# Optimization experiments

Measured on AMD Instinct MI355X. Metric: run time of the kernel, lower is better.

## Reference

```python
import jax, jax.numpy as jnp
import numpy as np

B, T, D, H, W = 128, 1024, 32, 64, 128
C = D + 1            # control_size = data_size + 1
O = H * C            # cvf MLP output size


def _linear_params(k, out_f, in_f):
    lim = 1.0 / np.sqrt(in_f)
    kw, kb = jax.random.split(k)
    Wm = jax.random.uniform(kw, (out_f, in_f), minval=-lim, maxval=lim, dtype=jnp.float32)
    b = jax.random.uniform(kb, (out_f,), minval=-lim, maxval=lim, dtype=jnp.float32)
    return Wm, b


def setup_inputs() -> dict:
    key = jax.random.key(0)
    ks = jax.random.split(key, 8)
    # initial MLP: (D+1) -> W -> W -> H, relu hidden
    iW0, ib0 = _linear_params(ks[0], W, D + 1)
    iW1, ib1 = _linear_params(ks[1], W, W)
    iW2, ib2 = _linear_params(ks[2], H, W)
    # cvf MLP: (H+1) -> W -> W -> H*C, lipswish hidden, tanh final
    vW0, vb0 = _linear_params(ks[3], W, H + 1)
    vW1, vb1 = _linear_params(ks[4], W, W)
    vW2, vb2 = _linear_params(ks[5], O, W)
    # readout: H -> 1
    rW, rb = _linear_params(ks[6], 1, H)
    ts = jnp.arange(T, dtype=jnp.float32)
    ys = jax.random.normal(ks[7], (B, T, D), dtype=jnp.float32)
    return dict(ts=ts, ys=ys,
                iW0=iW0, ib0=ib0, iW1=iW1, ib1=ib1, iW2=iW2, ib2=ib2,
                vW0=vW0, vb0=vb0, vW1=vb1 * 0 + vW1, vb1=vb1, vW2=vW2, vb2=vb2,
                rW=rW, rb=rb)


def _lipswish(x):
    return 0.909 * jax.nn.silu(x)


def reference(ts, ys, iW0, ib0, iW1, ib1, iW2, ib2,
              vW0, vb0, vW1, vb1, vW2, vb2, rW, rb):
    b, t_len, d = ys.shape
    h = iW2.shape[0]
    c = d + 1

    def initial_mlp(x):  # [B, D+1] -> [B, H]
        z = jax.nn.relu(x @ iW0.T + ib0)
        z = jax.nn.relu(z @ iW1.T + ib1)
        return z @ iW2.T + ib2

    def vf(t, y):  # scalar t, y [B,H] -> [B,H,C]
        inp = jnp.concatenate([jnp.full((y.shape[0], 1), t, y.dtype), y], axis=1)
        z = _lipswish(inp @ vW0.T + vb0)
        z = _lipswish(z @ vW1.T + vb1)
        out = jnp.tanh(z @ vW2.T + vb2)
        return out.reshape(y.shape[0], h, c)

    # control path values x(t_i) = [t_i, y_i]; no NaNs so interpolation fixups are no-ops
    xs = jnp.concatenate([jnp.broadcast_to(ts[None, :, None], (b, t_len, 1)), ys], axis=2)  # [B,T,C]
    y0 = initial_mlp(xs[:, 0])
    vf0 = vf(ts[0], y0)

    # constant step dt=1 aligned with grid -> control increments are consecutive diffs
    dxs = jnp.swapaxes(xs[:, 1:] - xs[:, :-1], 0, 1)  # [T-1,B,C]
    t1s = ts[1:]

    def step(carry, inp):
        y, yhat, v = carry
        t1, dx = inp
        # ReversibleHeun: yhat1 = 2*y - yhat + f(t0,yhat0)·dx ; y1 = y + 0.5*(f0+f1)·dx
        yhat1 = 2.0 * y - yhat + jnp.einsum('bhc,bc->bh', v, dx)
        v1 = vf(t1, yhat1)
        y1 = y + 0.5 * jnp.einsum('bhc,bc->bh', v + v1, dx)
        return (y1, yhat1, v1), None

    (yT, _, _), _ = jax.lax.scan(step, (y0, y0, vf0), (t1s, dxs))
    return yT @ rW.T + rb  # [B,1]
```

## Files before the change

### kernel.cpp

```cpp
#include <hip/hip_runtime.h>
#include <math.h>

constexpr int kB  = 128;
constexpr int kT  = 1024;
constexpr int kD  = 32;
constexpr int kH  = 64;
constexpr int kW  = 128;
constexpr int kC  = kD + 1;
constexpr int kO  = kH * kC;
constexpr int kIN = kH + 1;
constexpr int BLOCK = 1024;

constexpr int WS_W2  = 0;
constexpr int WS_W1  = 135168;
constexpr int WS_W0  = 143360;
constexpr int WS_SC2 = 147584;
constexpr int WS_SC1 = 149696;
constexpr int WS_SC0 = 149824;
constexpr int WS_TOT = 149952;

__device__ __forceinline__ float fast_sigmoid(float x) { return 1.0f / (1.0f + __expf(-x)); }
__device__ __forceinline__ float lipswish_f(float x)   { return 0.909f * x * fast_sigmoid(x); }
__device__ __forceinline__ float fast_tanh(float x) {
    float ax = fabsf(x);
    float e  = __expf(2.0f * ax);
    float r  = 1.0f - 2.0f / (e + 1.0f);
    return copysignf(r, x);
}
__device__ __forceinline__ float dot4(float4 a, float4 b) {
    return a.x * b.x + a.y * b.y + a.z * b.z + a.w * b.w;
}
__device__ __forceinline__ float fma2i(unsigned u, float z0, float z1, float acc) {
    int lo = (int)(short)(u & 0xffffu);
    int hi = ((int)u) >> 16;
    acc += (float)lo * z0 + (float)hi * z1;
    return acc;
}
__device__ __forceinline__ float fma8i(uint4 u, float4 zl, float4 zh, float acc) {
    acc = fma2i(u.x, zl.x, zl.y, acc);
    acc = fma2i(u.y, zl.z, zl.w, acc);
    acc = fma2i(u.z, zh.x, zh.y, acc);
    acc = fma2i(u.w, zh.z, zh.w, acc);
    return acc;
}
__device__ __forceinline__ int q15(float w, float inv) {
    float q = rintf(w * inv);
    q = fmaxf(-32767.0f, fminf(32767.0f, q));
    return (int)q;
}
__device__ __forceinline__ unsigned pack16(int a, int b) {
    return ((unsigned)a & 0xffffu) | ((unsigned)b << 16);
}

__global__ __launch_bounds__(64)
void prep_kernel(const float* __restrict__ vW0, const float* __restrict__ vW1,
                 const float* __restrict__ vW2, unsigned* __restrict__ ws)
{
    const int row  = blockIdx.x;
    const int lane = threadIdx.x;
    float* scf = (float*)ws;

    if (row < kO) {
        const float* src = vW2 + (size_t)row * kW;
        float m = fmaxf(fabsf(src[lane]), fabsf(src[lane + 64]));
        #pragma unroll
        for (int s = 1; s < 64; s <<= 1) m = fmaxf(m, __shfl_xor(m, s));
        float inv = (m > 0.0f) ? 32767.0f / m : 0.0f;
        if (lane == 0) scf[WS_SC2 + row] = (m > 0.0f) ? m / 32767.0f : 0.0f;
        int w = lane;
        unsigned pk = pack16(q15(src[2 * w], inv), q15(src[2 * w + 1], inv));
        int R = row >> 6, r = row & 63, q = w >> 2, e = w & 3;
        ws[WS_W2 + (((R * 16 + q) * 64 + r) << 2) + e] = pk;
    } else if (row < kO + kW) {
        int r = row - kO;
        const float* src = vW1 + (size_t)r * kW;
        float m = fmaxf(fabsf(src[lane]), fabsf(src[lane + 64]));
        #pragma unroll
        for (int s = 1; s < 64; s <<= 1) m = fmaxf(m, __shfl_xor(m, s));
        float inv = (m > 0.0f) ? 32767.0f / m : 0.0f;
        if (lane == 0) scf[WS_SC1 + r] = (m > 0.0f) ? m / 32767.0f : 0.0f;
        int w = lane;
        ws[WS_W1 + r * 64 + w] = pack16(q15(src[2 * w], inv), q15(src[2 * w + 1], inv));
    } else {
        int r = row - kO - kW;
        const float* src = vW0 + (size_t)r * kIN;
        float m = fabsf(src[lane]);
        if (lane == 0) m = fmaxf(m, fabsf(src[64]));
        #pragma unroll
        for (int s = 1; s < 64; s <<= 1) m = fmaxf(m, __shfl_xor(m, s));
        float inv = (m > 0.0f) ? 32767.0f / m : 0.0f;
        if (lane == 0) scf[WS_SC0 + r] = (m > 0.0f) ? m / 32767.0f : 0.0f;
        if (lane < 33) {
            int c0 = 2 * lane, c1 = 2 * lane + 1;
            int qa = q15(src[c0], inv);
            int qb = (c1 < kIN) ? q15(src[c1], inv) : 0;
            ws[WS_W0 + r * 33 + lane] = pack16(qa, qb);
        }
    }
}

template <int QI>
__global__ __launch_bounds__(BLOCK)
void cde_kernel(
    const float* __restrict__ ts,  const float* __restrict__ ys,
    const float* __restrict__ iW0, const float* __restrict__ ib0,
    const float* __restrict__ iW1, const float* __restrict__ ib1,
    const float* __restrict__ iW2, const float* __restrict__ ib2,
    const float* __restrict__ vW0, const float* __restrict__ vb0,
    const float* __restrict__ vW1, const float* __restrict__ vb1,
    const float* __restrict__ vW2, const float* __restrict__ vb2,
    const float* __restrict__ rW,  const float* __restrict__ rb,
    const unsigned* __restrict__ wsb,
    float* __restrict__ out)
{
    const int b  = blockIdx.x;
    const int t  = threadIdx.x;
    const int r8 = t >> 3;
    const int g  = t & 7;
    const int wv = t >> 6;
    const int ln = t & 63;

    __shared__ __align__(16) float s_v[kO];
    __shared__ __align__(16) float s_z1[kW], s_z2[kW];
    __shared__ __align__(16) float s_inp[kIN + 1];
    __shared__ float s_y[kH], s_yhat[kH], s_e[kH];
    __shared__ float s_dx[kC];

    const float*    ysb   = ys + (size_t)b * kT * kD;
    const uint4*    wsW2q = (const uint4*)(wsb + WS_W2);
    const unsigned* wsW1  = wsb + WS_W1;
    const unsigned* wsW0  = wsb + WS_W0;
    const float*    scf   = (const float*)wsb;

    const float bA  = vb2[t];
    const float bB  = vb2[t + 1024];
    const float bTl = (t < 512) ? vb2[2048 + r8] : 0.0f;
    const float b0r = vb0[r8];
    const float b1r = vb1[r8];
    const float sA  = QI ? scf[WS_SC2 + t] : 0.0f;
    const float sB  = QI ? scf[WS_SC2 + t + 1024] : 0.0f;
    const float sTl = (QI && t < 512) ? scf[WS_SC2 + 2048 + r8] : 0.0f;
    const float s0r = QI ? scf[WS_SC0 + r8] : 0.0f;
    const float s1r = QI ? scf[WS_SC1 + r8] : 0.0f;

    float x_reg = 0.0f, x_next = 0.0f;
    if (t < kC) {
        x_reg  = (t == 0) ? ts[0] : ysb[t - 1];
        x_next = (t == 0) ? ts[1] : ysb[kD + (t - 1)];
        s_dx[t] = x_reg;
    }
    if (t == 0) s_inp[kIN] = 0.0f;
    __syncthreads();

    if (t < kW) {
        const float* wrow = iW0 + t * kC;
        float acc = ib0[t];
        #pragma unroll
        for (int c = 0; c < kC; c++) acc += wrow[c] * s_dx[c];
        s_z1[t] = fmaxf(acc, 0.0f);
    }
    __syncthreads();
    if (t < kW) {
        const float4* wr = (const float4*)(iW1 + t * kW);
        const float4* z4 = (const float4*)s_z1;
        float acc = ib1[t];
        #pragma unroll 8
        for (int q = 0; q < kW / 4; q++) acc += dot4(wr[q], z4[q]);
        s_z2[t] = fmaxf(acc, 0.0f);
    }
    __syncthreads();
    if (t < kH) {
        const float4* wr = (const float4*)(iW2 + t * kW);
        const float4* z4 = (const float4*)s_z2;
        float acc = ib2[t];
        #pragma unroll 8
        for (int q = 0; q < kW / 4; q++) acc += dot4(wr[q], z4[q]);
        s_y[t] = acc; s_yhat[t] = acc;
        s_inp[1 + t] = acc;
    }
    if (t == 0) s_inp[0] = x_reg;
    __syncthreads();

    for (int i = 0; i < kT; i++) {
        {
            float acc = 0.0f;
            if (QI) {
                const unsigned* rowp = wsW0 + r8 * 33;
                #pragma unroll
                for (int m = 0; m < 5; m++) {
                    int p = g + 8 * m;
                    if (p < 33) acc = fma2i(rowp[p], s_inp[2 * p], s_inp[2 * p + 1], acc);
                }
            } else {
                const float* rowp = vW0 + r8 * kIN;
                #pragma unroll
                for (int m = 0; m < 5; m++) {
                    int p = g + 8 * m;
                    if (p < 33) {
                        float w0 = rowp[2 * p];
                        float w1 = (2 * p + 1 < kIN) ? rowp[2 * p + 1] : 0.0f;
                        acc += w0 * s_inp[2 * p] + w1 * s_inp[2 * p + 1];
                    }
                }
            }
            acc += __shfl_xor(acc, 1);
            acc += __shfl_xor(acc, 2);
            acc += __shfl_xor(acc, 4);
            if (g == 0) s_z1[r8] = lipswish_f(b0r + (QI ? s0r * acc : acc));
        }
        __syncthreads();
        {
            float acc = 0.0f;
            #pragma unroll
            for (int m = 0; m < 2; m++) {
                int ch = g + 8 * m;
                int c0 = 8 * ch;
                const float4* z4 = (const float4*)(s_z1 + c0);
                float4 za = z4[0], zb = z4[1];
                if (QI) {
                    uint4 u = *(const uint4*)(wsW1 + r8 * 64 + 4 * ch);
                    acc = fma8i(u, za, zb, acc);
                } else {
                    const float* wr = vW1 + r8 * kW + c0;
                    acc += dot4(*(const float4*)wr, za) + dot4(*(const float4*)(wr + 4), zb);
                }
            }
            acc += __shfl_xor(acc, 1);
            acc += __shfl_xor(acc, 2);
            acc += __shfl_xor(acc, 4);
            if (g == 0) s_z2[r8] = lipswish_f(b1r + (QI ? s1r * acc : acc));
        }
        __syncthreads();
        {
            float acc0 = 0.0f, acc1 = 0.0f;
            if (QI) {
                const uint4* pA = wsW2q + (size_t)(wv * 16) * 64 + ln;
                const uint4* pB = wsW2q + (size_t)((wv + 16) * 16) * 64 + ln;
                #pragma unroll 2
                for (int m = 0; m < 8; m++) {
                    const float4* z4 = (const float4*)(s_z2 + 16 * m);
                    float4 z0 = z4[0], z1 = z4[1], z2 = z4[2], z3 = z4[3];
                    uint4 a0 = pA[(2 * m) * 64],     a1 = pA[(2 * m + 1) * 64];
                    uint4 c0 = pB[(2 * m) * 64],     c1 = pB[(2 * m + 1) * 64];
                    acc0 = fma8i(a0, z0, z1, acc0);
                    acc0 = fma8i(a1, z2, z3, acc0);
                    acc1 = fma8i(c0, z0, z1, acc1);
                    acc1 = fma8i(c1, z2, z3, acc1);
                }
                s_v[t]        = fast_tanh(bA + sA * acc0);
                s_v[t + 1024] = fast_tanh(bB + sB * acc1);
            } else {
                #pragma unroll 2
                for (int m = 0; m < 8; m++) {
                    const float4* z4 = (const float4*)(s_z2 + 16 * m);
                    float4 z0 = z4[0], z1 = z4[1], z2 = z4[2], z3 = z4[3];
                    const float4* rA = (const float4*)(vW2 + (size_t)t * kW + 16 * m);
                    const float4* rB = (const float4*)(vW2 + (size_t)(t + 1024) * kW + 16 * m);
                    acc0 += dot4(rA[0], z0) + dot4(rA[1], z1) + dot4(rA[2], z2) + dot4(rA[3], z3);
                    acc1 += dot4(rB[0], z0) + dot4(rB[1], z1) + dot4(rB[2], z2) + dot4(rB[3], z3);
                }
                s_v[t]        = fast_tanh(bA + acc0);
                s_v[t + 1024] = fast_tanh(bB + acc1);
            }
        }
        if (t < 512) {
            int c0 = 16 * g;
            const float4* z4 = (const float4*)(s_z2 + c0);
            float4 z0 = z4[0], z1 = z4[1], z2 = z4[2], z3 = z4[3];
            float acc = 0.0f;
            if (QI) {
                uint4 u0 = wsW2q[(size_t)(32 * 16 + 2 * g) * 64 + r8];
                uint4 u1 = wsW2q[(size_t)(32 * 16 + 2 * g + 1) * 64 + r8];
                acc = fma8i(u0, z0, z1, acc);
                acc = fma8i(u1, z2, z3, acc);
            } else {
                const float4* wr = (const float4*)(vW2 + (size_t)(2048 + r8) * kW + c0);
                acc += dot4(wr[0], z0) + dot4(wr[1], z1) + dot4(wr[2], z2) + dot4(wr[3], z3);
            }
            acc += __shfl_xor(acc, 1);
            acc += __shfl_xor(acc, 2);
            acc += __shfl_xor(acc, 4);
            if (g == 0) s_v[2048 + r8] = fast_tanh(bTl + (QI ? sTl * acc : acc));
        }
        __syncthreads();

        if (i > 0 && t < kH) {
            const float* vr = s_v + t * kC;
            float acc = 0.0f;
            #pragma unroll
            for (int c = 0; c < kC; c++) acc += vr[c] * s_dx[c];
            s_y[t] += 0.5f * (s_e[t] + acc);
        }
        __syncthreads();

        if (i < kT - 1) {
            if (t < kC) {
                float xi = x_next;
                s_dx[t] = xi - x_reg;
                x_reg = xi;
                if (i + 2 < kT)
                    x_next = (t == 0) ? ts[i + 2] : ysb[(size_t)(i + 2) * kD + (t - 1)];
            }
            __syncthreads();
            if (t < kH) {
                const float* vr = s_v + t * kC;
                float e = 0.0f;
                #pragma unroll
                for (int c = 0; c < kC; c++) e += vr[c] * s_dx[c];
                s_e[t] = e;
                float yh = 2.0f * s_y[t] - s_yhat[t] + e;
                s_yhat[t] = yh;
                s_inp[1 + t] = yh;
            }
            if (t == 0) s_inp[0] = x_reg;
            __syncthreads();
        }
    }

    __syncthreads();
    if (t == 0) {
        float acc = rb[0];
        #pragma unroll
        for (int h = 0; h < kH; h++) acc += s_y[h] * rW[h];
        out[b] = acc;
    }
}

extern "C" void kernel_launch(void* const* d_in, const int* in_sizes, int n_in,
                              void* d_out, int out_size, void* d_ws, size_t ws_size,
                              hipStream_t stream)
{
    const float* ts  = (const float*)d_in[0];
    const float* ys  = (const float*)d_in[1];
    const float* iW0 = (const float*)d_in[2];
    const float* ib0 = (const float*)d_in[3];
    const float* iW1 = (const float*)d_in[4];
    const float* ib1 = (const float*)d_in[5];
    const float* iW2 = (const float*)d_in[6];
    const float* ib2 = (const float*)d_in[7];
    const float* vW0 = (const float*)d_in[8];
    const float* vb0 = (const float*)d_in[9];
    const float* vW1 = (const float*)d_in[10];
    const float* vb1 = (const float*)d_in[11];
    const float* vW2 = (const float*)d_in[12];
    const float* vb2 = (const float*)d_in[13];
    const float* rW  = (const float*)d_in[14];
    const float* rb  = (const float*)d_in[15];
    float* out = (float*)d_out;
    unsigned* ws = (unsigned*)d_ws;

    if (ws_size >= (size_t)WS_TOT * 4) {
        hipLaunchKernelGGL(prep_kernel, dim3(kO + kW + kW), dim3(64), 0, stream,
                           vW0, vW1, vW2, ws);
        hipLaunchKernelGGL((cde_kernel<1>), dim3(kB), dim3(BLOCK), 0, stream,
                           ts, ys, iW0, ib0, iW1, ib1, iW2, ib2,
                           vW0, vb0, vW1, vb1, vW2, vb2, rW, rb, ws, out);
    } else {
        hipLaunchKernelGGL((cde_kernel<0>), dim3(kB), dim3(BLOCK), 0, stream,
                           ts, ys, iW0, ib0, iW1, ib1, iW2, ib2,
                           vW0, vb0, vW1, vb1, vW2, vb2, rW, rb, ws, out);
    }
}
```

Measured before the change: 6.456 ms.

## Batch 16 sequences per block and run MLP layers on int8 MFMA

The main kernel now processes 16 batch elements per block, using 8 blocks instead of 128. Each MLP layer of the vector field runs as int8 16x16x64 MFMA ops. Weights are split into hi/lo bytes and activations into three bytes under a dynamic per-step scale, which emulates high-precision integer matmul. Results for v are stored as 16-bit quantized values in shared memory. This moves the per-step work from scalar FMA GEMVs onto matrix cores and reuses weights across the batch. The cost is much lower parallelism across CUs, extra quantization and reduction syncs each step, and a risk of precision loss.

```diff
diff --git a/kernel.cpp b/kernel.cpp
--- a/kernel.cpp
+++ b/kernel.cpp
@@ -1,5 +1,7 @@
 #include <hip/hip_runtime.h>
 #include <math.h>
+
+typedef __attribute__((ext_vector_type(4))) int i32x4;
 
 constexpr int kB  = 128;
 constexpr int kT  = 1024;
@@ -9,15 +11,19 @@
 constexpr int kC  = kD + 1;
 constexpr int kO  = kH * kC;
 constexpr int kIN = kH + 1;
+constexpr int BPB   = 16;
+constexpr int NBLK  = kB / BPB;
 constexpr int BLOCK = 1024;
 
-constexpr int WS_W2  = 0;
-constexpr int WS_W1  = 135168;
-constexpr int WS_W0  = 143360;
-constexpr int WS_SC2 = 147584;
-constexpr int WS_SC1 = 149696;
-constexpr int WS_SC0 = 149824;
+constexpr int W2B  = 0;
+constexpr int W1B  = 540672;
+constexpr int W0B  = 573440;
+constexpr int SC2W = 147456;
+constexpr int SC1W = 149568;
+constexpr int SC0W = 149696;
 constexpr int WS_TOT = 149952;
+
+constexpr float QA = 8323072.0f;
 
 __device__ __forceinline__ float fast_sigmoid(float x) { return 1.0f / (1.0f + __expf(-x)); }
 __device__ __forceinline__ float lipswish_f(float x)   { return 0.909f * x * fast_sigmoid(x); }
@@ -30,77 +36,97 @@
 __device__ __forceinline__ float dot4(float4 a, float4 b) {
     return a.x * b.x + a.y * b.y + a.z * b.z + a.w * b.w;
 }
-__device__ __forceinline__ float fma2i(unsigned u, float z0, float z1, float acc) {
-    int lo = (int)(short)(u & 0xffffu);
-    int hi = ((int)u) >> 16;
-    acc += (float)lo * z0 + (float)hi * z1;
-    return acc;
-}
-__device__ __forceinline__ float fma8i(uint4 u, float4 zl, float4 zh, float acc) {
-    acc = fma2i(u.x, zl.x, zl.y, acc);
-    acc = fma2i(u.y, zl.z, zl.w, acc);
-    acc = fma2i(u.z, zh.x, zh.y, acc);
-    acc = fma2i(u.w, zh.z, zh.w, acc);
-    return acc;
-}
-__device__ __forceinline__ int q15(float w, float inv) {
-    float q = rintf(w * inv);
-    q = fmaxf(-32767.0f, fminf(32767.0f, q));
+__device__ __forceinline__ void split16(int q, int& lo, int& hi) {
+    lo = (int)(signed char)(q & 0xFF);
+    hi = (q - lo) >> 8;
+}
+__device__ __forceinline__ int q15c(float v, float inv) {
+    float q = rintf(v * inv);
+    q = fmaxf(-32511.0f, fminf(32511.0f, q));
     return (int)q;
 }
-__device__ __forceinline__ unsigned pack16(int a, int b) {
-    return ((unsigned)a & 0xffffu) | ((unsigned)b << 16);
+__device__ __forceinline__ int q24c(float v, float inv) {
+    float q = rintf(v * inv);
+    q = fmaxf(-8355711.0f, fminf(8355711.0f, q));
+    return (int)q;
+}
+__device__ __forceinline__ void split24(int q, int& a0, int& a1, int& a2) {
+    a0 = (int)(signed char)(q & 0xFF);
+    int r = (q - a0) >> 8;
+    a1 = (int)(signed char)(r & 0xFF);
+    a2 = (r - a1) >> 8;
+}
+__device__ __forceinline__ i32x4 mmi8(uint4 a, uint4 b, i32x4 c) {
+    union { uint4 u; i32x4 v; } ua, ub;
+    ua.u = a; ub.u = b;
+    return __builtin_amdgcn_mfma_i32_16x16x64_i8(ua.v, ub.v, c, 0, 0, 0);
 }
 
 __global__ __launch_bounds__(64)
 void prep_kernel(const float* __restrict__ vW0, const float* __restrict__ vW1,
                  const float* __restrict__ vW2, unsigned* __restrict__ ws)
 {
-    const int row  = blockIdx.x;
-    const int lane = threadIdx.x;
+    const int row = blockIdx.x, ln = threadIdx.x;
+    char*  wb  = (char*)ws;
     float* scf = (float*)ws;
 
     if (row < kO) {
         const float* src = vW2 + (size_t)row * kW;
-        float m = fmaxf(fabsf(src[lane]), fabsf(src[lane + 64]));
+        float m = fmaxf(fabsf(src[ln]), fabsf(src[ln + 64]));
         #pragma unroll
         for (int s = 1; s < 64; s <<= 1) m = fmaxf(m, __shfl_xor(m, s));
-        float inv = (m > 0.0f) ? 32767.0f / m : 0.0f;
-        if (lane == 0) scf[WS_SC2 + row] = (m > 0.0f) ? m / 32767.0f : 0.0f;
-        int w = lane;
-        unsigned pk = pack16(q15(src[2 * w], inv), q15(src[2 * w + 1], inv));
-        int R = row >> 6, r = row & 63, q = w >> 2, e = w & 3;
-        ws[WS_W2 + (((R * 16 + q) * 64 + r) << 2) + e] = pk;
+        float inv = (m > 0.f) ? 32511.f / m : 0.f;
+        if (ln == 0) scf[SC2W + row] = (m > 0.f) ? m / 32511.f : 0.f;
+        const int M = row >> 4, ri = row & 15;
+        #pragma unroll
+        for (int h = 0; h < 2; h++) {
+            int c = ln + 64 * h;
+            int q = q15c(src[c], inv);
+            int lo, hi; split16(q, lo, hi);
+            int lp = ((c & 63) >> 4) * 16 + ri, j = c & 15;
+            size_t base = (size_t)W2B + (size_t)((M * 2 + h) * 2) * 1024 + lp * 16 + j;
+            wb[base]        = (char)hi;
+            wb[base + 1024] = (char)lo;
+        }
     } else if (row < kO + kW) {
-        int r = row - kO;
+        const int r = row - kO;
         const float* src = vW1 + (size_t)r * kW;
-        float m = fmaxf(fabsf(src[lane]), fabsf(src[lane + 64]));
+        float m = fmaxf(fabsf(src[ln]), fabsf(src[ln + 64]));
         #pragma unroll
         for (int s = 1; s < 64; s <<= 1) m = fmaxf(m, __shfl_xor(m, s));
-        float inv = (m > 0.0f) ? 32767.0f / m : 0.0f;
-        if (lane == 0) scf[WS_SC1 + r] = (m > 0.0f) ? m / 32767.0f : 0.0f;
-        int w = lane;
-        ws[WS_W1 + r * 64 + w] = pack16(q15(src[2 * w], inv), q15(src[2 * w + 1], inv));
+        float inv = (m > 0.f) ? 32511.f / m : 0.f;
+        if (ln == 0) scf[SC1W + r] = (m > 0.f) ? m / 32511.f : 0.f;
+        const int M = r >> 4, ri = r & 15;
+        #pragma unroll
+        for (int h = 0; h < 2; h++) {
+            int c = ln + 64 * h;
+            int q = q15c(src[c], inv);
+            int lo, hi; split16(q, lo, hi);
+            int lp = ((c & 63) >> 4) * 16 + ri, j = c & 15;
+            size_t base = (size_t)W1B + (size_t)((M * 2 + h) * 2) * 1024 + lp * 16 + j;
+            wb[base]        = (char)hi;
+            wb[base + 1024] = (char)lo;
+        }
     } else {
-        int r = row - kO - kW;
+        const int r = row - kO - kW;
         const float* src = vW0 + (size_t)r * kIN;
-        float m = fabsf(src[lane]);
-        if (lane == 0) m = fmaxf(m, fabsf(src[64]));
+        float m = fabsf(src[ln + 1]);
         #pragma unroll
         for (int s = 1; s < 64; s <<= 1) m = fmaxf(m, __shfl_xor(m, s));
-        float inv = (m > 0.0f) ? 32767.0f / m : 0.0f;
-        if (lane == 0) scf[WS_SC0 + r] = (m > 0.0f) ? m / 32767.0f : 0.0f;
-        if (lane < 33) {
-            int c0 = 2 * lane, c1 = 2 * lane + 1;
-            int qa = q15(src[c0], inv);
-            int qb = (c1 < kIN) ? q15(src[c1], inv) : 0;
-            ws[WS_W0 + r * 33 + lane] = pack16(qa, qb);
-        }
-    }
-}
-
-template <int QI>
-__global__ __launch_bounds__(BLOCK)
+        float inv = (m > 0.f) ? 32511.f / m : 0.f;
+        if (ln == 0) scf[SC0W + r] = (m > 0.f) ? m / 32511.f : 0.f;
+        const int M = r >> 4, ri = r & 15;
+        int k = ln;
+        int q = q15c(src[k + 1], inv);
+        int lo, hi; split16(q, lo, hi);
+        int lp = (k >> 4) * 16 + ri, j = k & 15;
+        size_t base = (size_t)W0B + (size_t)(M * 2) * 1024 + lp * 16 + j;
+        wb[base]        = (char)hi;
+        wb[base + 1024] = (char)lo;
+    }
+}
+
+__global__ __attribute__((amdgpu_flat_work_group_size(1024, 1024), amdgpu_waves_per_eu(4, 4)))
 void cde_kernel(
     const float* __restrict__ ts,  const float* __restrict__ ys,
     const float* __restrict__ iW0, const float* __restrict__ ib0,
@@ -113,12 +139,317 @@
     const unsigned* __restrict__ wsb,
     float* __restrict__ out)
 {
+    const int t   = threadIdx.x;
+    const int wv  = t >> 6;
+    const int ln  = t & 63;
+    const int bq  = ln & 15;
+    const int bG0 = blockIdx.x * BPB;
+
+    __shared__ __align__(16) uint4 s_inpq[3][64];
+    __shared__ __align__(16) uint4 s_z1q[2][3][64];
+    __shared__ __align__(16) uint4 s_z2q[2][3][64];
+    __shared__ __align__(16) unsigned short s_v[16 * 2178];
+    __shared__ float s_y[16 * 65], s_yh[16 * 65], s_e[16 * 65];
+    __shared__ float s_dx[2][16][34];
+    __shared__ float s_red[16];
+    __shared__ float s_scales[4];
+
+    const uint4* w2q = (const uint4*)wsb;
+    const uint4* w1q = (const uint4*)((const char*)wsb + W1B);
+    const uint4* w0q = (const uint4*)((const char*)wsb + W0B);
+    const float* scf = (const float*)wsb;
+
+    {
+        float* s_x0 = (float*)s_v;
+        float* s_zA = (float*)s_v + 528;
+        float* s_zB = (float*)s_v + 2576;
+        for (int idx = t; idx < BPB * kC; idx += BLOCK) {
+            int b = idx / kC, c = idx - b * kC;
+            s_x0[idx] = (c == 0) ? ts[0] : ys[(size_t)(bG0 + b) * kT * kD + (c - 1)];
+        }
+        __syncthreads();
+        {
+            const int row = t & 127, bb = t >> 7;
+            float a0 = ib0[row], a1 = a0;
+            const float* wr = iW0 + (size_t)row * kC;
+            for (int c = 0; c < kC; c++) {
+                float w = wr[c];
+                a0 += w * s_x0[bb * kC + c];
+                a1 += w * s_x0[(bb + 8) * kC + c];
+            }
+            s_zA[bb * kW + row]       = fmaxf(a0, 0.f);
+            s_zA[(bb + 8) * kW + row] = fmaxf(a1, 0.f);
+        }
+        __syncthreads();
+        {
+            const int row = t & 127, bb = t >> 7;
+            float a0 = ib1[row], a1 = a0;
+            const float* wr = iW1 + (size_t)row * kW;
+            for (int c = 0; c < kW; c++) {
+                float w = wr[c];
+                a0 += w * s_zA[bb * kW + c];
+                a1 += w * s_zA[(bb + 8) * kW + c];
+            }
+            s_zB[bb * kW + row]       = fmaxf(a0, 0.f);
+            s_zB[(bb + 8) * kW + row] = fmaxf(a1, 0.f);
+        }
+        __syncthreads();
+        float a = 0.f;
+        {
+            const int row = t & 63, b = t >> 6;
+            a = ib2[row];
+            const float* wr = iW2 + (size_t)row * kW;
+            for (int c = 0; c < kW; c++) a += wr[c] * s_zB[b * kW + c];
+            float am = fabsf(a);
+            #pragma unroll
+            for (int s = 1; s < 64; s <<= 1) am = fmaxf(am, __shfl_xor(am, s));
+            if (ln == 0) s_red[wv] = am;
+        }
+        __syncthreads();
+        {
+            const int row = t & 63, b = t >> 6;
+            s_y[b * 65 + row]  = a;
+            s_yh[b * 65 + row] = a;
+            float gm = s_red[0];
+            #pragma unroll
+            for (int k = 1; k < 16; k++) gm = fmaxf(gm, s_red[k]);
+            float inv = (gm > 0.f) ? QA / gm : 0.f;
+            int q = q24c(a, inv);
+            int a0p, a1p, a2p; split24(q, a0p, a1p, a2p);
+            int lp = (row >> 4) * 16 + b, jj = row & 15;
+            char* ib = (char*)s_inpq;
+            ib[lp * 16 + jj]        = (char)a2p;
+            ib[1024 + lp * 16 + jj] = (char)a1p;
+            ib[2048 + lp * 16 + jj] = (char)a0p;
+            if (t == 0) s_scales[0] = gm / QA;
+        }
+    }
+    int bd = 0, cd = 0;
+    float x_reg = 0.f, x_next = 0.f;
+    const float* yptr = nullptr;
+    const bool isdx = (t < BPB * kC);
+    if (isdx) {
+        bd = t / kC; cd = t - bd * kC;
+        if (cd == 0) { x_reg = ts[0]; x_next = ts[1]; }
+        else {
+            const float* pp = ys + (size_t)(bG0 + bd) * kT * kD + (cd - 1);
+            x_reg = pp[0]; x_next = pp[kD]; yptr = pp + 2 * kD;
+        }
+        s_dx[0][bd][cd] = 0.f;
+    }
+    __syncthreads();
+
+    const i32x4 zz = {0, 0, 0, 0};
+
+    for (int i = 0; i < kT; i++) {
+        float z1v[4] = {0.f, 0.f, 0.f, 0.f};
+        float amA = 0.f;
+        if (wv >= 8) {
+            const int M = wv - 8;
+            uint4 wh = w0q[M * 128 + ln], wl = w0q[M * 128 + 64 + ln];
+            uint4 i2 = s_inpq[0][ln], i1 = s_inpq[1][ln], i0 = s_inpq[2][ln];
+            i32x4 A = mmi8(wh, i2, zz);
+            i32x4 B = mmi8(wh, i1, zz); B = mmi8(wl, i2, B);
+            i32x4 C = mmi8(wh, i0, zz); C = mmi8(wl, i1, C);
+            const float sinp = s_scales[0];
+            const float tc = ts[i];
+            const int r0 = 16 * M + 4 * (ln >> 4);
+            #pragma unroll
+            for (int r = 0; r < 4; r++) {
+                int rw = r0 + r;
+                float raw = 16777216.f * (float)A[r] + 65536.f * (float)B[r] + 256.f * (float)C[r];
+                float pre = scf[SC0W + rw] * sinp * raw + vW0[(size_t)rw * kIN] * tc + vb0[rw];
+                z1v[r] = lipswish_f(pre);
+                amA = fmaxf(amA, fabsf(z1v[r]));
+            }
+            #pragma unroll
+            for (int s = 1; s < 64; s <<= 1) amA = fmaxf(amA, __shfl_xor(amA, s));
+            if (ln == 0) s_red[wv] = amA;
+        }
+        if (isdx && i + 1 < kT) {
+            float dxv = x_next - x_reg; x_reg = x_next;
+            s_dx[(i + 1) & 1][bd][cd] = dxv;
+            if (i + 2 < kT) {
+                if (cd == 0) x_next = ts[i + 2];
+                else { x_next = *yptr; yptr += kD; }
+            }
+        }
+        __syncthreads();
+
+        if (wv >= 8) {
+            float gm = fmaxf(fmaxf(fmaxf(s_red[8], s_red[9]), fmaxf(s_red[10], s_red[11])),
+                             fmaxf(fmaxf(s_red[12], s_red[13]), fmaxf(s_red[14], s_red[15])));
+            float inv = (gm > 0.f) ? QA / gm : 0.f;
+            if (wv == 8 && ln == 0) s_scales[1] = gm / QA;
+            const int M = wv - 8;
+            char* zb = (char*)s_z1q;
+            #pragma unroll
+            for (int r = 0; r < 4; r++) {
+                int k = 16 * M + 4 * (ln >> 4) + r;
+                int q = q24c(z1v[r], inv);
+                int a0p, a1p, a2p; split24(q, a0p, a1p, a2p);
+                int kc = k >> 6, lp = ((k & 63) >> 4) * 16 + bq, jj = k & 15;
+                int off = kc * 3072 + lp * 16 + jj;
+                zb[off]        = (char)a2p;
+                zb[off + 1024] = (char)a1p;
+                zb[off + 2048] = (char)a0p;
+            }
+        }
+        __syncthreads();
+
+        float z2v[4] = {0.f, 0.f, 0.f, 0.f};
+        if (wv < 8) {
+            const uint4* p = w1q + wv * 256 + ln;
+            uint4 wh0 = p[0], wl0 = p[64], wh1 = p[128], wl1 = p[192];
+            uint4 x20 = s_z1q[0][0][ln], x10 = s_z1q[0][1][ln], x00 = s_z1q[0][2][ln];
+            uint4 x21 = s_z1q[1][0][ln], x11 = s_z1q[1][1][ln], x01 = s_z1q[1][2][ln];
+            i32x4 A = mmi8(wh0, x20, zz); A = mmi8(wh1, x21, A);
+            i32x4 B = mmi8(wh0, x10, zz); B = mmi8(wl0, x20, B);
+            B = mmi8(wh1, x11, B); B = mmi8(wl1, x21, B);
+            i32x4 C = mmi8(wh0, x00, zz); C = mmi8(wl0, x10, C);
+            C = mmi8(wh1, x01, C); C = mmi8(wl1, x11, C);
+            const float sz1 = s_scales[1];
+            const int r0 = 16 * wv + 4 * (ln >> 4);
+            float amC = 0.f;
+            #pragma unroll
+            for (int r = 0; r < 4; r++) {
+                int rw = r0 + r;
+                float raw = 16777216.f * (float)A[r] + 65536.f * (float)B[r] + 256.f * (float)C[r];
+                float pre = scf[SC1W + rw] * sz1 * raw + vb1[rw];
+                z2v[r] = lipswish_f(pre);
+                amC = fmaxf(amC, fabsf(z2v[r]));
+            }
+            #pragma unroll
+            for (int s = 1; s < 64; s <<= 1) amC = fmaxf(amC, __shfl_xor(amC, s));
+            if (ln == 0) s_red[wv] = amC;
+        }
+        __syncthreads();
+
+        if (wv < 8) {
+            float gm = fmaxf(fmaxf(fmaxf(s_red[0], s_red[1]), fmaxf(s_red[2], s_red[3])),
+                             fmaxf(fmaxf(s_red[4], s_red[5]), fmaxf(s_red[6], s_red[7])));
+            float inv = (gm > 0.f) ? QA / gm : 0.f;
+            if (wv == 0 && ln == 0) s_scales[2] = gm / QA;
+            char* zb = (char*)s_z2q;
+            #pragma unroll
+            for (int r = 0; r < 4; r++) {
+                int k = 16 * wv + 4 * (ln >> 4) + r;
+                int q = q24c(z2v[r], inv);
+                int a0p, a1p, a2p; split24(q, a0p, a1p, a2p);
+                int kc = k >> 6, lp = ((k & 63) >> 4) * 16 + bq, jj = k & 15;
+                int off = kc * 3072 + lp * 16 + jj;
+                zb[off]        = (char)a2p;
+                zb[off + 1024] = (char)a1p;
+                zb[off + 2048] = (char)a0p;
+            }
+        }
+        __syncthreads();
+
+        {
+            const uint4 y20 = s_z2q[0][0][ln], y10 = s_z2q[0][1][ln], y00 = s_z2q[0][2][ln];
+            const uint4 y21 = s_z2q[1][0][ln], y11 = s_z2q[1][1][ln], y01 = s_z2q[1][2][ln];
+            const float sz2 = s_scales[2];
+            const int nj = (wv < 4) ? 9 : 8;
+            for (int j = 0; j < nj; j++) {
+                const int Mt = wv + 16 * j;
+                const uint4* p = w2q + (size_t)Mt * 256 + ln;
+                uint4 wh0 = p[0], wl0 = p[64], wh1 = p[128], wl1 = p[192];
+                i32x4 A = mmi8(wh0, y20, zz); A = mmi8(wh1, y21, A);
+                i32x4 B = mmi8(wh0, y10, zz); B = mmi8(wl0, y20, B);
+                B = mmi8(wh1, y11, B); B = mmi8(wl1, y21, B);
+                i32x4 C = mmi8(wh0, y00, zz); C = mmi8(wl0, y10, C);
+                C = mmi8(wh1, y01, C); C = mmi8(wl1, y11, C);
+                const int r0 = 16 * Mt + 4 * (ln >> 4);
+                #pragma unroll
+                for (int r = 0; r < 4; r++) {
+                    int rw = r0 + r;
+                    float raw = 16777216.f * (float)A[r] + 65536.f * (float)B[r] + 256.f * (float)C[r];
+                    float val = fast_tanh(fmaf(scf[SC2W + rw] * sz2, raw, vb2[rw]));
+                    int q = (int)rintf(val * 32511.f);
+                    int hq = (int)((unsigned)rw / 33u);
+                    int cq = rw - hq * 33;
+                    s_v[bq * 2178 + hq * 34 + cq] = (unsigned short)q;
+                }
+            }
+        }
+        __syncthreads();
+
+        float yh_new = 0.f, amF = 0.f;
+        {
+            const int be = t & 15, he = t >> 4;
+            const unsigned* vp32 = (const unsigned*)(s_v + be * 2178 + he * 34);
+            const float* dx0 = &s_dx[i & 1][be][0];
+            const float* dx1 = &s_dx[(i + 1) & 1][be][0];
+            float E0 = 0.f, E1 = 0.f;
+            #pragma unroll
+            for (int qd = 0; qd < 16; qd++) {
+                unsigned u = vp32[qd];
+                float v0 = (float)(short)(u & 0xFFFFu);
+                float v1 = (float)(short)(u >> 16);
+                E0 += v0 * dx0[2 * qd] + v1 * dx0[2 * qd + 1];
+                E1 += v0 * dx1[2 * qd] + v1 * dx1[2 * qd + 1];
+            }
+            {
+                float v32 = (float)(short)((const unsigned short*)vp32)[32];
+                E0 += v32 * dx0[32]; E1 += v32 * dx1[32];
+            }
+            E0 *= (1.f / 32511.f); E1 *= (1.f / 32511.f);
+            const int id = be * 65 + he;
+            if (i > 0) s_y[id] += 0.5f * (s_e[id] + E0);
+            if (i < kT - 1) {
+                s_e[id] = E1;
+                yh_new = 2.f * s_y[id] - s_yh[id] + E1;
+                s_yh[id] = yh_new;
+                amF = fabsf(yh_new);
+            }
+        }
+        #pragma unroll
+        for (int s = 1; s < 64; s <<= 1) amF = fmaxf(amF, __shfl_xor(amF, s));
+        if (ln == 0) s_red[wv] = amF;
+        __syncthreads();
+
+        if (i < kT - 1) {
+            const int be = t & 15, he = t >> 4;
+            float gm = s_red[0];
+            #pragma unroll
+            for (int k = 1; k < 16; k++) gm = fmaxf(gm, s_red[k]);
+            float inv = (gm > 0.f) ? QA / gm : 0.f;
+            int q = q24c(yh_new, inv);
+            int a0p, a1p, a2p; split24(q, a0p, a1p, a2p);
+            int lp = (he >> 4) * 16 + be, jj = he & 15;
+            char* ib = (char*)s_inpq;
+            ib[lp * 16 + jj]        = (char)a2p;
+            ib[1024 + lp * 16 + jj] = (char)a1p;
+            ib[2048 + lp * 16 + jj] = (char)a0p;
+            if (t == 0) s_scales[0] = gm / QA;
+        }
+        __syncthreads();
+    }
+
+    if (t < BPB) {
+        float a = rb[0];
+        #pragma unroll
+        for (int h = 0; h < kH; h++) a += s_y[t * 65 + h] * rW[h];
+        out[bG0 + t] = a;
+    }
+}
+
+__global__ __launch_bounds__(BLOCK)
+void cde_mono0(
+    const float* __restrict__ ts,  const float* __restrict__ ys,
+    const float* __restrict__ iW0, const float* __restrict__ ib0,
+    const float* __restrict__ iW1, const float* __restrict__ ib1,
+    const float* __restrict__ iW2, const float* __restrict__ ib2,
+    const float* __restrict__ vW0, const float* __restrict__ vb0,
+    const float* __restrict__ vW1, const float* __restrict__ vb1,
+    const float* __restrict__ vW2, const float* __restrict__ vb2,
+    const float* __restrict__ rW,  const float* __restrict__ rb,
+    float* __restrict__ out)
+{
     const int b  = blockIdx.x;
     const int t  = threadIdx.x;
     const int r8 = t >> 3;
     const int g  = t & 7;
-    const int wv = t >> 6;
-    const int ln = t & 63;
 
     __shared__ __align__(16) float s_v[kO];
     __shared__ __align__(16) float s_z1[kW], s_z2[kW];
@@ -126,22 +457,10 @@
     __shared__ float s_y[kH], s_yhat[kH], s_e[kH];
     __shared__ float s_dx[kC];
 
-    const float*    ysb   = ys + (size_t)b * kT * kD;
-    const uint4*    wsW2q = (const uint4*)(wsb + WS_W2);
-    const unsigned* wsW1  = wsb + WS_W1;
-    const unsigned* wsW0  = wsb + WS_W0;
-    const float*    scf   = (const float*)wsb;
-
+    const float* ysb = ys + (size_t)b * kT * kD;
     const float bA  = vb2[t];
     const float bB  = vb2[t + 1024];
     const float bTl = (t < 512) ? vb2[2048 + r8] : 0.0f;
-    const float b0r = vb0[r8];
-    const float b1r = vb1[r8];
-    const float sA  = QI ? scf[WS_SC2 + t] : 0.0f;
-    const float sB  = QI ? scf[WS_SC2 + t + 1024] : 0.0f;
-    const float sTl = (QI && t < 512) ? scf[WS_SC2 + 2048 + r8] : 0.0f;
-    const float s0r = QI ? scf[WS_SC0 + r8] : 0.0f;
-    const float s1r = QI ? scf[WS_SC1 + r8] : 0.0f;
 
     float x_reg = 0.0f, x_next = 0.0f;
     if (t < kC) {
@@ -151,7 +470,6 @@
     }
     if (t == 0) s_inp[kIN] = 0.0f;
     __syncthreads();
-
     if (t < kW) {
         const float* wrow = iW0 + t * kC;
         float acc = ib0[t];
@@ -184,29 +502,20 @@
     for (int i = 0; i < kT; i++) {
         {
             float acc = 0.0f;
-            if (QI) {
-                const unsigned* rowp = wsW0 + r8 * 33;
-                #pragma unroll
-                for (int m = 0; m < 5; m++) {
-                    int p = g + 8 * m;
-                    if (p < 33) acc = fma2i(rowp[p], s_inp[2 * p], s_inp[2 * p + 1], acc);
-                }
-            } else {
-                const float* rowp = vW0 + r8 * kIN;
-                #pragma unroll
-                for (int m = 0; m < 5; m++) {
-                    int p = g + 8 * m;
-                    if (p < 33) {
-                        float w0 = rowp[2 * p];
-                        float w1 = (2 * p + 1 < kIN) ? rowp[2 * p + 1] : 0.0f;
-                        acc += w0 * s_inp[2 * p] + w1 * s_inp[2 * p + 1];
-                    }
+            const float* rowp = vW0 + r8 * kIN;
+            #pragma unroll
+            for (int m = 0; m < 5; m++) {
+                int p = g + 8 * m;
+                if (p < 33) {
+                    float w0 = rowp[2 * p];
+                    float w1 = (2 * p + 1 < kIN) ? rowp[2 * p + 1] : 0.0f;
+                    acc += w0 * s_inp[2 * p] + w1 * s_inp[2 * p + 1];
                 }
             }
             acc += __shfl_xor(acc, 1);
             acc += __shfl_xor(acc, 2);
             acc += __shfl_xor(acc, 4);
-            if (g == 0) s_z1[r8] = lipswish_f(b0r + (QI ? s0r * acc : acc));
+            if (g == 0) s_z1[r8] = lipswish_f(vb0[r8] + acc);
         }
         __syncthreads();
         {
@@ -214,76 +523,40 @@
             #pragma unroll
             for (int m = 0; m < 2; m++) {
                 int ch = g + 8 * m;
-                int c0 = 8 * ch;
-                const float4* z4 = (const float4*)(s_z1 + c0);
-                float4 za = z4[0], zb = z4[1];
-                if (QI) {
-                    uint4 u = *(const uint4*)(wsW1 + r8 * 64 + 4 * ch);
-                    acc = fma8i(u, za, zb, acc);
-                } else {
-                    const float* wr = vW1 + r8 * kW + c0;
-                    acc += dot4(*(const float4*)wr, za) + dot4(*(const float4*)(wr + 4), zb);
-                }
+                const float4* z4 = (const float4*)(s_z1 + 8 * ch);
+                const float* wr = vW1 + r8 * kW + 8 * ch;
+                acc += dot4(*(const float4*)wr, z4[0]) + dot4(*(const float4*)(wr + 4), z4[1]);
             }
             acc += __shfl_xor(acc, 1);
             acc += __shfl_xor(acc, 2);
             acc += __shfl_xor(acc, 4);
-            if (g == 0) s_z2[r8] = lipswish_f(b1r + (QI ? s1r * acc : acc));
+            if (g == 0) s_z2[r8] = lipswish_f(vb1[r8] + acc);
         }
         __syncthreads();
         {
             float acc0 = 0.0f, acc1 = 0.0f;
-            if (QI) {
-                const uint4* pA = wsW2q + (size_t)(wv * 16) * 64 + ln;
-                const uint4* pB = wsW2q + (size_t)((wv + 16) * 16) * 64 + ln;
-                #pragma unroll 2
-                for (int m = 0; m < 8; m++) {
-                    const float4* z4 = (const float4*)(s_z2 + 16 * m);
-                    float4 z0 = z4[0], z1 = z4[1], z2 = z4[2], z3 = z4[3];
-                    uint4 a0 = pA[(2 * m) * 64],     a1 = pA[(2 * m + 1) * 64];
-                    uint4 c0 = pB[(2 * m) * 64],     c1 = pB[(2 * m + 1) * 64];
-                    acc0 = fma8i(a0, z0, z1, acc0);
-                    acc0 = fma8i(a1, z2, z3, acc0);
-                    acc1 = fma8i(c0, z0, z1, acc1);
-                    acc1 = fma8i(c1, z2, z3, acc1);
-                }
-                s_v[t]        = fast_tanh(bA + sA * acc0);
-                s_v[t + 1024] = fast_tanh(bB + sB * acc1);
-            } else {
-                #pragma unroll 2
-                for (int m = 0; m < 8; m++) {
-                    const float4* z4 = (const float4*)(s_z2 + 16 * m);
-                    float4 z0 = z4[0], z1 = z4[1], z2 = z4[2], z3 = z4[3];
-                    const float4* rA = (const float4*)(vW2 + (size_t)t * kW + 16 * m);
-                    const float4* rB = (const float4*)(vW2 + (size_t)(t + 1024) * kW + 16 * m);
-                    acc0 += dot4(rA[0], z0) + dot4(rA[1], z1) + dot4(rA[2], z2) + dot4(rA[3], z3);
-                    acc1 += dot4(rB[0], z0) + dot4(rB[1], z1) + dot4(rB[2], z2) + dot4(rB[3], z3);
-                }
-                s_v[t]        = fast_tanh(bA + acc0);
-                s_v[t + 1024] = fast_tanh(bB + acc1);
-            }
+            #pragma unroll 2
+            for (int m = 0; m < 8; m++) {
+                const float4* z4 = (const float4*)(s_z2 + 16 * m);
+                float4 z0 = z4[0], z1 = z4[1], z2 = z4[2], z3 = z4[3];
+                const float4* rA = (const float4*)(vW2 + (size_t)t * kW + 16 * m);
+                const float4* rB = (const float4*)(vW2 + (size_t)(t + 1024) * kW + 16 * m);
+                acc0 += dot4(rA[0], z0) + dot4(rA[1], z1) + dot4(rA[2], z2) + dot4(rA[3], z3);
+                acc1 += dot4(rB[0], z0) + dot4(rB[1], z1) + dot4(rB[2], z2) + dot4(rB[3], z3);
+            }
+            s_v[t]        = fast_tanh(bA + acc0);
+            s_v[t + 1024] = fast_tanh(bB + acc1);
         }
         if (t < 512) {
-            int c0 = 16 * g;
-            const float4* z4 = (const float4*)(s_z2 + c0);
-            float4 z0 = z4[0], z1 = z4[1], z2 = z4[2], z3 = z4[3];
-            float acc = 0.0f;
-            if (QI) {
-                uint4 u0 = wsW2q[(size_t)(32 * 16 + 2 * g) * 64 + r8];
-                uint4 u1 = wsW2q[(size_t)(32 * 16 + 2 * g + 1) * 64 + r8];
-                acc = fma8i(u0, z0, z1, acc);
-                acc = fma8i(u1, z2, z3, acc);
-            } else {
-                const float4* wr = (const float4*)(vW2 + (size_t)(2048 + r8) * kW + c0);
-                acc += dot4(wr[0], z0) + dot4(wr[1], z1) + dot4(wr[2], z2) + dot4(wr[3], z3);
-            }
+            const float4* z4 = (const float4*)(s_z2 + 16 * g);
+            const float4* wr = (const float4*)(vW2 + (size_t)(2048 + r8) * kW + 16 * g);
+            float acc = dot4(wr[0], z4[0]) + dot4(wr[1], z4[1]) + dot4(wr[2], z4[2]) + dot4(wr[3], z4[3]);
             acc += __shfl_xor(acc, 1);
             acc += __shfl_xor(acc, 2);
             acc += __shfl_xor(acc, 4);
-            if (g == 0) s_v[2048 + r8] = fast_tanh(bTl + (QI ? sTl * acc : acc));
-        }
-        __syncthreads();
-
+            if (g == 0) s_v[2048 + r8] = fast_tanh(bTl + acc);
+        }
+        __syncthreads();
         if (i > 0 && t < kH) {
             const float* vr = s_v + t * kC;
             float acc = 0.0f;
@@ -292,7 +565,6 @@
             s_y[t] += 0.5f * (s_e[t] + acc);
         }
         __syncthreads();
-
         if (i < kT - 1) {
             if (t < kC) {
                 float xi = x_next;
@@ -316,7 +588,6 @@
             __syncthreads();
         }
     }
-
     __syncthreads();
     if (t == 0) {
         float acc = rb[0];
@@ -346,18 +617,17 @@
     const float* vb2 = (const float*)d_in[13];
     const float* rW  = (const float*)d_in[14];
     const float* rb  = (const float*)d_in[15];
-    float* out = (float*)d_out;
-    unsigned* ws = (unsigned*)d_ws;
 
     if (ws_size >= (size_t)WS_TOT * 4) {
         hipLaunchKernelGGL(prep_kernel, dim3(kO + kW + kW), dim3(64), 0, stream,
-                           vW0, vW1, vW2, ws);
-        hipLaunchKernelGGL((cde_kernel<1>), dim3(kB), dim3(BLOCK), 0, stream,
+                           vW0, vW1, vW2, (unsigned*)d_ws);
+        hipLaunchKernelGGL(cde_kernel, dim3(NBLK), dim3(BLOCK), 0, stream,
                            ts, ys, iW0, ib0, iW1, ib1, iW2, ib2,
-                           vW0, vb0, vW1, vb1, vW2, vb2, rW, rb, ws, out);
+                           vW0, vb0, vW1, vb1, vW2, vb2, rW, rb,
+                           (const unsigned*)d_ws, (float*)d_out);
     } else {
-        hipLaunchKernelGGL((cde_kernel<0>), dim3(kB), dim3(BLOCK), 0, stream,
+        hipLaunchKernelGGL(cde_mono0, dim3(kB), dim3(BLOCK), 0, stream,
                            ts, ys, iW0, ib0, iW1, ib1, iW2, ib2,
-                           vW0, vb0, vW1, vb1, vW2, vb2, rW, rb, ws, out);
-    }
-}
+                           vW0, vb0, vW1, vb1, vW2, vb2, rW, rb, (float*)d_out);
+    }
+}
```

Result: slower. 15.13 ms (+134.4%).
